# Performance work log

Hardware: AMD Instinct MI355X
Metric: run time of the kernel (lower is better)

## Reference

```python
import jax, jax.numpy as jnp
import numpy as np

SCALING = 16.0 / 8.0  # alpha / rank
GAMMA = 1.0
EPS = 1e-12


def setup_inputs() -> dict:
    key = jax.random.key(0)
    ks = jax.random.split(key, 8)
    B, T, H, O = 4, 2048, 4096, 4096
    E_tot, E_act, r = 16, 4, 8
    return {
        "x": jax.random.normal(ks[0], (B, T, H), jnp.float32),
        "W_base": jax.random.normal(ks[1], (O, H), jnp.float32) * 0.02,
        "b_base": jax.random.normal(ks[2], (O,), jnp.float32) * 0.02,
        "lora_A": jax.random.normal(ks[3], (E_tot, r, H), jnp.float32) * 0.02,
        "lora_B": jax.random.normal(ks[4], (E_tot, O, r), jnp.float32) * 0.02,
        "router_W": jax.random.normal(ks[5], (E_tot, H), jnp.float32) * 0.02,
        "router_b": jax.random.normal(ks[6], (E_tot,), jnp.float32) * 0.02,
        "domain_prior": jax.random.uniform(ks[7], (E_tot,), jnp.float32),
        "active": jnp.arange(E_act, dtype=jnp.int32),
    }


def reference(x, W_base, b_base, lora_A, lora_B, router_W, router_b, domain_prior, active):
    # Base linear: [B,T,H] @ [H,O] -> [B,T,O]
    y = jnp.einsum('bth,oh->bto', x, W_base) + b_base
    # Gather active experts' low-rank factors
    A = lora_A[active]   # [E, r, H]
    Bm = lora_B[active]  # [E, O, r]
    # Grouped low-rank GEMMs (dropout is identity at inference)
    z = jnp.einsum('bth,erh->bter', x, A)            # [B,T,E,r]
    contribs = jnp.einsum('bter,eor->bteo', z, Bm) * SCALING  # [B,T,E,O]
    # Token router logits over all experts, restricted to active set
    logits = jnp.einsum('bth,eh->bte', x, router_W) + router_b  # [B,T,E_tot]
    logits = logits[..., active]                                 # [B,T,E]
    prior = domain_prior[active]                                 # [E]
    alpha = jax.nn.softmax(jnp.log(prior + EPS) + logits / GAMMA, axis=-1)  # [B,T,E]
    return y + jnp.einsum('bteo,bte->bto', contribs, alpha)
```

## Files before the change

kernel.cpp:

```cpp
#include <hip/hip_runtime.h>
#include <hip/hip_bf16.h>


typedef _Float16 f16x8 __attribute__((ext_vector_type(8)));
typedef float    f32x4 __attribute__((ext_vector_type(4)));

constexpr int H  = 4096;
constexpr int O  = 4096;
constexpr int KP = 4160;
constexpr int EA = 4;
constexpr float SCALING_F = 2.0f;

typedef const __attribute__((address_space(1))) void gvoid;
typedef __attribute__((address_space(3))) void svoid;

__device__ inline void gload16(const void* g, void* s) {
  __builtin_amdgcn_global_load_lds((gvoid*)g, (svoid*)s, 16, 0, 0);
}

__global__ __launch_bounds__(256) void convert_w3_kernel(
    const float* __restrict__ W, const float* __restrict__ lora_B,
    const float* __restrict__ lora_A, const float* __restrict__ router_W,
    const int* __restrict__ active, _Float16* __restrict__ wh,
    _Float16* __restrict__ vh) {
  const int bid = blockIdx.x;
  const int tid = threadIdx.x;
  if (bid < O) {
    const int o = bid;
    const float* wrow = W + (size_t)o * H;
    _Float16* dstrow = wh + (size_t)o * KP;
    for (int g = tid; g < 520; g += 256) {
      const int k = g * 8;
      float v[8];
      if (k < H) {
        float4 a = *(const float4*)(wrow + k), b = *(const float4*)(wrow + k + 4);
        v[0] = a.x; v[1] = a.y; v[2] = a.z; v[3] = a.w;
        v[4] = b.x; v[5] = b.y; v[6] = b.z; v[7] = b.w;
      } else if (k < H + 32) {
        const int e = (k - H) >> 3;
        const float* s = lora_B + ((size_t)active[e] * O + o) * 8;
        float4 a = *(const float4*)s, b = *(const float4*)(s + 4);
        v[0] = a.x; v[1] = a.y; v[2] = a.z; v[3] = a.w;
        v[4] = b.x; v[5] = b.y; v[6] = b.z; v[7] = b.w;
      } else {
#pragma unroll
        for (int i = 0; i < 8; ++i) v[i] = 0.f;
      }
      f16x8 h;
#pragma unroll
      for (int i = 0; i < 8; ++i) h[i] = (_Float16)v[i];
      *(f16x8*)(dstrow + k) = h;
    }
  } else {
    const int j = bid - O;
    const float* src = nullptr;
    if (j < 32)      src = lora_A + (size_t)(active[j >> 3] * 8 + (j & 7)) * H;
    else if (j < 36) src = router_W + (size_t)active[j - 32] * H;
    _Float16* dstrow = vh + (size_t)j * H;
    for (int g = tid; g < 512; g += 256) {
      const int k = g * 8;
      f16x8 h;
      if (src) {
        float4 a = *(const float4*)(src + k), b = *(const float4*)(src + k + 4);
        h[0] = (_Float16)a.x; h[1] = (_Float16)a.y;
        h[2] = (_Float16)a.z; h[3] = (_Float16)a.w;
        h[4] = (_Float16)b.x; h[5] = (_Float16)b.y;
        h[6] = (_Float16)b.z; h[7] = (_Float16)b.w;
      } else {
#pragma unroll
        for (int i = 0; i < 8; ++i) h[i] = (_Float16)0.f;
      }
      *(f16x8*)(dstrow + k) = h;
    }
  }
}

constexpr int TM = 16, KC = 128, NCH = H / KC;

__global__ __launch_bounds__(256) void router_fused3_kernel(
    const float* __restrict__ x, const _Float16* __restrict__ vh,
    const float* __restrict__ router_b, const float* __restrict__ prior,
    const int* __restrict__ active, _Float16* __restrict__ xh) {
  __shared__ _Float16 As[TM * KC];
  __shared__ _Float16 Vs[48 * KC];
  __shared__ float zred[4][TM][48];
  const int tid  = threadIdx.x;
  const int lane = tid & 63;
  const int w    = tid >> 6;
  const long t0  = (long)blockIdx.x * TM;
  const int row  = tid >> 4;
  const int c8   = tid & 15;
  const int r15  = lane & 15;
  const int kg   = lane >> 4;

  const float* xrow = x + (t0 + row) * H + c8 * 8;
  _Float16*    xhrow = xh + (t0 + row) * KP + c8 * 8;
  _Float16*    asdst = As + row * KC + (c8 ^ row) * 8;

  f32x4 acc[3];
  const f32x4 zero = {0.f, 0.f, 0.f, 0.f};
  acc[0] = zero; acc[1] = zero; acc[2] = zero;

  float4 xa = *(const float4*)(xrow);
  float4 xb = *(const float4*)(xrow + 4);

  for (int t = 0; t < NCH; ++t) {
    const int k0 = t * KC;
    float4 na, nb;
    if (t + 1 < NCH) {
      na = *(const float4*)(xrow + k0 + KC);
      nb = *(const float4*)(xrow + k0 + KC + 4);
    }
    __syncthreads();
    f16x8 h;
    h[0] = (_Float16)xa.x; h[1] = (_Float16)xa.y;
    h[2] = (_Float16)xa.z; h[3] = (_Float16)xa.w;
    h[4] = (_Float16)xb.x; h[5] = (_Float16)xb.y;
    h[6] = (_Float16)xb.z; h[7] = (_Float16)xb.w;
    *(f16x8*)asdst = h;
    *(f16x8*)(xhrow + k0) = h;
#pragma unroll
    for (int j = 0; j < 3; ++j) {
      const int sv   = tid + 256 * j;
      const int vrow = sv >> 4;
      const int vs8  = sv & 15;
      gload16(vh + (size_t)vrow * H + k0 + ((vs8 ^ (vrow & 15)) * 8),
              Vs + sv * 8);
    }
    __syncthreads();
    const int slot = ((w * 4 + kg) ^ r15) * 8;
    f16x8 a = *(const f16x8*)(As + r15 * KC + slot);
#pragma unroll
    for (int nf = 0; nf < 3; ++nf) {
      const int vr = nf * 16 + r15;
      f16x8 b = *(const f16x8*)(Vs + vr * KC + (((w * 4 + kg) ^ (vr & 15)) * 8));
      acc[nf] = __builtin_amdgcn_mfma_f32_16x16x32_f16(a, b, acc[nf], 0, 0, 0);
    }
    xa = na; xb = nb;
  }

#pragma unroll
  for (int nf = 0; nf < 3; ++nf)
#pragma unroll
    for (int r = 0; r < 4; ++r)
      zred[w][kg * 4 + r][nf * 16 + r15] = acc[nf][r];
  __syncthreads();

  float s[3];
#pragma unroll
  for (int j = 0; j < 3; ++j) {
    const int sl = tid + 256 * j;
    const int tt = sl / 48, jj = sl % 48;
    s[j] = zred[0][tt][jj] + zred[1][tt][jj] + zred[2][tt][jj] + zred[3][tt][jj];
  }
  __syncthreads();
#pragma unroll
  for (int j = 0; j < 3; ++j) {
    const int sl = tid + 256 * j;
    zred[0][sl / 48][sl % 48] = s[j];
  }
  __syncthreads();

  if (tid < TM * EA) {
    const int tt = tid >> 2, e = tid & 3;
    const float* zt = &zred[0][tt][0];
    float le[EA], mx = -1e30f;
#pragma unroll
    for (int e2 = 0; e2 < EA; ++e2) {
      const int ae = active[e2];
      le[e2] = logf(prior[ae] + 1e-12f) + zt[32 + e2] + router_b[ae];
      mx = fmaxf(mx, le[e2]);
    }
    float sum = 0.f;
#pragma unroll
    for (int e2 = 0; e2 < EA; ++e2) sum += expf(le[e2] - mx);
    const float a = expf(le[e] - mx) / sum * SCALING_F;
    f16x8 ch, zz;
#pragma unroll
    for (int r = 0; r < 8; ++r) {
      ch[r] = (_Float16)(a * zt[e * 8 + r]);
      zz[r] = (_Float16)0.f;
    }
    _Float16* xr = xh + (t0 + tt) * KP + H;
    *(f16x8*)(xr + e * 8) = ch;
    *(f16x8*)(xr + 32 + e * 8) = zz;
  }
}

constexpr int BM = 128, BN = 128, BK = 64;

__global__ __launch_bounds__(256) void gemm_kernel(
    const _Float16* __restrict__ xh, const _Float16* __restrict__ wh,
    const float* __restrict__ b_base, float* __restrict__ out) {
  __shared__ _Float16 As[BM * BK];
  __shared__ _Float16 Ws[BN * BK];
  const int tid  = threadIdx.x;
  const int lane = tid & 63;
  const int wave = tid >> 6;
  const int bid = (int)blockIdx.x;
  const int swz = (bid & 7) * 256 + (bid >> 3);
  const int im = swz >> 5;
  const int in = swz & 31;
  const size_t trow0 = (size_t)im * BM;
  const size_t ocol0 = (size_t)in * BN;
  const int wr = wave >> 1, wc = wave & 1;

  f32x4 acc[4][4];
  const f32x4 zero = {0.f, 0.f, 0.f, 0.f};
#pragma unroll
  for (int m = 0; m < 4; ++m)
#pragma unroll
    for (int n = 0; n < 4; ++n) acc[m][n] = zero;

  const int srow  = lane >> 3;
  const int sslot = (lane & 7) ^ srow;
  const int r15 = lane & 15;
  const int kg  = lane >> 4;

  for (int step = 0; step < KP / BK; ++step) {
    const int k0 = step * BK;
    __syncthreads();
#pragma unroll
    for (int i = 0; i < 8; ++i) {
      const int ch  = wave + 4 * i;
      const int sub = ch & 15;
      const int row = sub * 8 + srow;
      if (ch < 16)
        gload16(xh + (trow0 + row) * KP + k0 + sslot * 8, As + sub * 512);
      else
        gload16(wh + (ocol0 + row) * KP + k0 + sslot * 8, Ws + sub * 512);
    }
    __syncthreads();
#pragma unroll
    for (int kk = 0; kk < 2; ++kk) {
      f16x8 a[4], b[4];
#pragma unroll
      for (int m = 0; m < 4; ++m) {
        const int row  = wr * 64 + m * 16 + r15;
        const int slot = (kk * 4 + kg) ^ (row & 7);
        a[m] = *(const f16x8*)(As + row * 64 + slot * 8);
      }
#pragma unroll
      for (int n = 0; n < 4; ++n) {
        const int row  = wc * 64 + n * 16 + r15;
        const int slot = (kk * 4 + kg) ^ (row & 7);
        b[n] = *(const f16x8*)(Ws + row * 64 + slot * 8);
      }
#pragma unroll
      for (int m = 0; m < 4; ++m)
#pragma unroll
        for (int n = 0; n < 4; ++n)
          acc[m][n] = __builtin_amdgcn_mfma_f32_16x16x32_f16(a[m], b[n], acc[m][n], 0, 0, 0);
    }
  }
#pragma unroll
  for (int n = 0; n < 4; ++n) {
    const size_t col = ocol0 + wc * 64 + n * 16 + r15;
    const float bb = b_base[col];
#pragma unroll
    for (int m = 0; m < 4; ++m) {
      const size_t row = trow0 + wr * 64 + m * 16 + kg * 4;
#pragma unroll
      for (int j = 0; j < 4; ++j)
        out[(row + j) * O + col] = acc[m][n][j] + bb;
    }
  }
}

extern "C" void kernel_launch(void* const* d_in, const int* in_sizes, int n_in,
                              void* d_out, int out_size, void* d_ws, size_t ws_size,
                              hipStream_t stream) {
  const float* x        = (const float*)d_in[0];
  const float* W_base   = (const float*)d_in[1];
  const float* b_base   = (const float*)d_in[2];
  const float* lora_A   = (const float*)d_in[3];
  const float* lora_B   = (const float*)d_in[4];
  const float* router_W = (const float*)d_in[5];
  const float* router_b = (const float*)d_in[6];
  const float* prior    = (const float*)d_in[7];
  const int*   active   = (const int*)d_in[8];
  float* out = (float*)d_out;

  const int M = in_sizes[0] / H;

  char* ws = (char*)d_ws;
  _Float16* xh = (_Float16*)ws;
  _Float16* wh = (_Float16*)(ws + (size_t)M * KP * 2);
  _Float16* vh = (_Float16*)(ws + (size_t)M * KP * 2 + (size_t)O * KP * 2);

  convert_w3_kernel<<<O + 48, 256, 0, stream>>>(W_base, lora_B, lora_A, router_W,
                                                active, wh, vh);
  router_fused3_kernel<<<M / TM, 256, 0, stream>>>(x, vh, router_b, prior, active, xh);
  gemm_kernel<<<(M / BM) * (O / BN), 256, 0, stream>>>(xh, wh, b_base, out);
}
```

Measured before the change: 604.7 us.

## Double-buffer GEMM LDS tiles and load router operands directly from global

The main GEMM now keeps two LDS buffers and issues the next tile's async global-to-LDS loads before computing the current one, with explicit vmcnt waits and barriers. This overlaps memory latency with MFMA work. The router kernel drops its LDS staging and reads x and the router/LoRA-A weights straight into MFMA fragments, removing per-chunk block barriers. The block-index swizzle for L2 locality is also removed, which may reduce cache reuse. LDS usage doubles, which could affect occupancy.

```diff
diff --git a/kernel.cpp b/kernel.cpp
--- a/kernel.cpp
+++ b/kernel.cpp
@@ -75,68 +75,42 @@
   }
 }
 
-constexpr int TM = 16, KC = 128, NCH = H / KC;
-
-__global__ __launch_bounds__(256) void router_fused3_kernel(
+__global__ __launch_bounds__(256) void router_fused4_kernel(
     const float* __restrict__ x, const _Float16* __restrict__ vh,
     const float* __restrict__ router_b, const float* __restrict__ prior,
     const int* __restrict__ active, _Float16* __restrict__ xh) {
-  __shared__ _Float16 As[TM * KC];
-  __shared__ _Float16 Vs[48 * KC];
-  __shared__ float zred[4][TM][48];
+  __shared__ float zred[4][16][48];
   const int tid  = threadIdx.x;
   const int lane = tid & 63;
   const int w    = tid >> 6;
-  const long t0  = (long)blockIdx.x * TM;
-  const int row  = tid >> 4;
-  const int c8   = tid & 15;
+  const long t0  = (long)blockIdx.x * 16;
   const int r15  = lane & 15;
   const int kg   = lane >> 4;
 
-  const float* xrow = x + (t0 + row) * H + c8 * 8;
-  _Float16*    xhrow = xh + (t0 + row) * KP + c8 * 8;
-  _Float16*    asdst = As + row * KC + (c8 ^ row) * 8;
+  const float*    xp  = x  + (t0 + r15) * H  + w * 32 + kg * 8;
+  _Float16*       xhp = xh + (t0 + r15) * KP + w * 32 + kg * 8;
+  const _Float16* vp  = vh + (size_t)r15 * H + w * 32 + kg * 8;
 
   f32x4 acc[3];
   const f32x4 zero = {0.f, 0.f, 0.f, 0.f};
   acc[0] = zero; acc[1] = zero; acc[2] = zero;
 
-  float4 xa = *(const float4*)(xrow);
-  float4 xb = *(const float4*)(xrow + 4);
-
-  for (int t = 0; t < NCH; ++t) {
-    const int k0 = t * KC;
-    float4 na, nb;
-    if (t + 1 < NCH) {
-      na = *(const float4*)(xrow + k0 + KC);
-      nb = *(const float4*)(xrow + k0 + KC + 4);
-    }
-    __syncthreads();
-    f16x8 h;
-    h[0] = (_Float16)xa.x; h[1] = (_Float16)xa.y;
-    h[2] = (_Float16)xa.z; h[3] = (_Float16)xa.w;
-    h[4] = (_Float16)xb.x; h[5] = (_Float16)xb.y;
-    h[6] = (_Float16)xb.z; h[7] = (_Float16)xb.w;
-    *(f16x8*)asdst = h;
-    *(f16x8*)(xhrow + k0) = h;
-#pragma unroll
-    for (int j = 0; j < 3; ++j) {
-      const int sv   = tid + 256 * j;
-      const int vrow = sv >> 4;
-      const int vs8  = sv & 15;
-      gload16(vh + (size_t)vrow * H + k0 + ((vs8 ^ (vrow & 15)) * 8),
-              Vs + sv * 8);
-    }
-    __syncthreads();
-    const int slot = ((w * 4 + kg) ^ r15) * 8;
-    f16x8 a = *(const f16x8*)(As + r15 * KC + slot);
+#pragma unroll 2
+  for (int c = 0; c < 32; ++c) {
+    const int ko = c * 128;
+    float4 v0 = *(const float4*)(xp + ko);
+    float4 v1 = *(const float4*)(xp + ko + 4);
+    f16x8 a;
+    a[0] = (_Float16)v0.x; a[1] = (_Float16)v0.y;
+    a[2] = (_Float16)v0.z; a[3] = (_Float16)v0.w;
+    a[4] = (_Float16)v1.x; a[5] = (_Float16)v1.y;
+    a[6] = (_Float16)v1.z; a[7] = (_Float16)v1.w;
+    *(f16x8*)(xhp + ko) = a;
 #pragma unroll
     for (int nf = 0; nf < 3; ++nf) {
-      const int vr = nf * 16 + r15;
-      f16x8 b = *(const f16x8*)(Vs + vr * KC + (((w * 4 + kg) ^ (vr & 15)) * 8));
+      f16x8 b = *(const f16x8*)(vp + (size_t)nf * 16 * H + ko);
       acc[nf] = __builtin_amdgcn_mfma_f32_16x16x32_f16(a, b, acc[nf], 0, 0, 0);
     }
-    xa = na; xb = nb;
   }
 
 #pragma unroll
@@ -161,7 +135,7 @@
   }
   __syncthreads();
 
-  if (tid < TM * EA) {
+  if (tid < 16 * EA) {
     const int tt = tid >> 2, e = tid & 3;
     const float* zt = &zred[0][tt][0];
     float le[EA], mx = -1e30f;
@@ -187,20 +161,19 @@
   }
 }
 
-constexpr int BM = 128, BN = 128, BK = 64;
+constexpr int BM = 128, BN = 128, BK = 64, NT = KP / BK;
 
 __global__ __launch_bounds__(256) void gemm_kernel(
     const _Float16* __restrict__ xh, const _Float16* __restrict__ wh,
     const float* __restrict__ b_base, float* __restrict__ out) {
-  __shared__ _Float16 As[BM * BK];
-  __shared__ _Float16 Ws[BN * BK];
+  __shared__ _Float16 As[2][BM * BK];
+  __shared__ _Float16 Ws[2][BN * BK];
   const int tid  = threadIdx.x;
   const int lane = tid & 63;
   const int wave = tid >> 6;
-  const int bid = (int)blockIdx.x;
-  const int swz = (bid & 7) * 256 + (bid >> 3);
-  const int im = swz >> 5;
-  const int in = swz & 31;
+  const int bid  = (int)blockIdx.x;
+  const int im = bid >> 5;
+  const int in = bid & 31;
   const size_t trow0 = (size_t)im * BM;
   const size_t ocol0 = (size_t)in * BN;
   const int wr = wave >> 1, wc = wave & 1;
@@ -217,42 +190,54 @@
   const int r15 = lane & 15;
   const int kg  = lane >> 4;
 
-  for (int step = 0; step < KP / BK; ++step) {
-    const int k0 = step * BK;
-    __syncthreads();
+  auto stage = [&](int b, int t) {
+    const int k0 = t * BK;
 #pragma unroll
     for (int i = 0; i < 8; ++i) {
       const int ch  = wave + 4 * i;
       const int sub = ch & 15;
       const int row = sub * 8 + srow;
       if (ch < 16)
-        gload16(xh + (trow0 + row) * KP + k0 + sslot * 8, As + sub * 512);
+        gload16(xh + (trow0 + row) * KP + k0 + sslot * 8, &As[b][sub * 512]);
       else
-        gload16(wh + (ocol0 + row) * KP + k0 + sslot * 8, Ws + sub * 512);
-    }
-    __syncthreads();
+        gload16(wh + (ocol0 + row) * KP + k0 + sslot * 8, &Ws[b][sub * 512]);
+    }
+  };
+
+  stage(0, 0);
+  for (int t = 0; t < NT; ++t) {
+    const int b = t & 1;
+    if (t + 1 < NT) {
+      stage(b ^ 1, t + 1);
+      asm volatile("s_waitcnt vmcnt(8)" ::: "memory");
+    } else {
+      asm volatile("s_waitcnt vmcnt(0)" ::: "memory");
+    }
+    __builtin_amdgcn_s_barrier();
 #pragma unroll
     for (int kk = 0; kk < 2; ++kk) {
-      f16x8 a[4], b[4];
+      f16x8 a[4], bfr[4];
 #pragma unroll
       for (int m = 0; m < 4; ++m) {
         const int row  = wr * 64 + m * 16 + r15;
         const int slot = (kk * 4 + kg) ^ (row & 7);
-        a[m] = *(const f16x8*)(As + row * 64 + slot * 8);
+        a[m] = *(const f16x8*)(&As[b][row * 64 + slot * 8]);
       }
 #pragma unroll
       for (int n = 0; n < 4; ++n) {
         const int row  = wc * 64 + n * 16 + r15;
         const int slot = (kk * 4 + kg) ^ (row & 7);
-        b[n] = *(const f16x8*)(Ws + row * 64 + slot * 8);
+        bfr[n] = *(const f16x8*)(&Ws[b][row * 64 + slot * 8]);
       }
 #pragma unroll
       for (int m = 0; m < 4; ++m)
 #pragma unroll
         for (int n = 0; n < 4; ++n)
-          acc[m][n] = __builtin_amdgcn_mfma_f32_16x16x32_f16(a[m], b[n], acc[m][n], 0, 0, 0);
-    }
-  }
+          acc[m][n] = __builtin_amdgcn_mfma_f32_16x16x32_f16(a[m], bfr[n], acc[m][n], 0, 0, 0);
+    }
+    __builtin_amdgcn_s_barrier();
+  }
+
 #pragma unroll
   for (int n = 0; n < 4; ++n) {
     const size_t col = ocol0 + wc * 64 + n * 16 + r15;
@@ -290,6 +275,6 @@
 
   convert_w3_kernel<<<O + 48, 256, 0, stream>>>(W_base, lora_B, lora_A, router_W,
                                                 active, wh, vh);
-  router_fused3_kernel<<<M / TM, 256, 0, stream>>>(x, vh, router_b, prior, active, xh);
+  router_fused4_kernel<<<M / 16, 256, 0, stream>>>(x, vh, router_b, prior, active, xh);
   gemm_kernel<<<(M / BM) * (O / BN), 256, 0, stream>>>(xh, wh, b_base, out);
 }
```

Result: no change. 612.5 us (+1.3%).
